# Optimization experiments

Hardware: AMD Instinct MI355X
Metric: run time of the kernel (lower is better)

## Reference

```python
import jax, jax.numpy as jnp
import numpy as np
from jax import lax

B, T, A, L, H, FD = 32, 64, 6, 32, 128, 256


def setup_inputs() -> dict:
    key = jax.random.key(0)
    ks = jax.random.split(key, 24)
    rn = lambda k, s, sc: jax.random.normal(k, s, jnp.float32) * sc
    return {
        "states": rn(ks[0], (B, T, 3, 64, 64), 1.0),
        "actions": rn(ks[1], (B, T, A), 1.0),
        # CNN encoder params (scale ~ 1/sqrt(fan_in))
        "c1_w": rn(ks[2], (32, 3, 4, 4), 0.14), "c1_b": rn(ks[3], (32,), 0.01),
        "c2_w": rn(ks[4], (64, 32, 4, 4), 0.044), "c2_b": rn(ks[5], (64,), 0.01),
        "c3_w": rn(ks[6], (128, 64, 4, 4), 0.031), "c3_b": rn(ks[7], (128,), 0.01),
        "c4_w": rn(ks[8], (256, 128, 4, 4), 0.022), "c4_b": rn(ks[9], (256,), 0.01),
        "fc_w": rn(ks[10], (FD, 256 * 4 * 4), 0.0156), "fc_b": rn(ks[11], (FD,), 0.01),
        # GRUCell params (torch layout: W_ih (3H, in), W_hh (3H, H))
        "gru_wih": rn(ks[12], (3 * H, L + A), 0.16), "gru_whh": rn(ks[13], (3 * H, H), 0.088),
        "gru_bih": rn(ks[14], (3 * H,), 0.01), "gru_bhh": rn(ks[15], (3 * H,), 0.01),
        "prior_w": rn(ks[16], (2 * L, H), 0.088), "prior_b": rn(ks[17], (2 * L,), 0.01),
        "post_w": rn(ks[18], (2 * L, H + FD), 0.05), "post_b": rn(ks[19], (2 * L,), 0.01),
        # reparameterization noise (randn_like in torch), one per (b, t)
        "eps": rn(ks[20], (B, T, L), 1.0),
    }


def _conv(x, w, b):
    # Conv2d(k=4, stride=2, pad=1), NCHW/OIHW
    y = lax.conv_general_dilated(x, w, window_strides=(2, 2),
                                 padding=[(1, 1), (1, 1)],
                                 dimension_numbers=("NCHW", "OIHW", "NCHW"))
    return jax.nn.relu(y + b[None, :, None, None])


def _encode(x, c1_w, c1_b, c2_w, c2_b, c3_w, c3_b, c4_w, c4_b, fc_w, fc_b):
    # x: (N, 3, 64, 64) -> (N, FD)
    x = _conv(x, c1_w, c1_b)
    x = _conv(x, c2_w, c2_b)
    x = _conv(x, c3_w, c3_b)
    x = _conv(x, c4_w, c4_b)  # (N, 256, 4, 4)
    x = x.reshape(x.shape[0], -1)
    return x @ fc_w.T + fc_b


def _gru_cell(x, h, wih, whh, bih, bhh):
    gi = x @ wih.T + bih
    gh = h @ whh.T + bhh
    i_r, i_z, i_n = jnp.split(gi, 3, axis=-1)
    h_r, h_z, h_n = jnp.split(gh, 3, axis=-1)
    r = jax.nn.sigmoid(i_r + h_r)
    z = jax.nn.sigmoid(i_z + h_z)
    n = jnp.tanh(i_n + r * h_n)
    return (1.0 - z) * n + z * h


def reference(states, actions, c1_w, c1_b, c2_w, c2_b, c3_w, c3_b, c4_w, c4_b,
              fc_w, fc_b, gru_wih, gru_whh, gru_bih, gru_bhh,
              prior_w, prior_b, post_w, post_b, eps):
    b, t = states.shape[0], states.shape[1]
    # encoder has no recurrent dependency: encode all frames at once
    feats = _encode(states.reshape(b * t, *states.shape[2:]),
                    c1_w, c1_b, c2_w, c2_b, c3_w, c3_b, c4_w, c4_b,
                    fc_w, fc_b).reshape(b, t, -1)  # (B, T, FD)

    def step(carry, inp):
        h, z = carry
        a_t, f_t, e_t = inp
        h = _gru_cell(jnp.concatenate([z, a_t], -1), h,
                      gru_wih, gru_whh, gru_bih, gru_bhh)
        mu_p, lv_p = jnp.split(h @ prior_w.T + prior_b, 2, axis=-1)
        mu_q, lv_q = jnp.split(jnp.concatenate([h, f_t], -1) @ post_w.T + post_b, 2, axis=-1)
        z = mu_q + jnp.exp(0.5 * lv_q) * e_t
        return (h, z), (mu_p, lv_p, mu_q, lv_q, h, z)

    h0 = jnp.zeros((b, gru_whh.shape[1]), states.dtype)
    z0 = jnp.zeros((b, prior_w.shape[0] // 2), states.dtype)
    xs = (jnp.swapaxes(actions, 0, 1), jnp.swapaxes(feats, 0, 1),
          jnp.swapaxes(eps, 0, 1))
    _, ys = lax.scan(step, (h0, z0), xs)
    # (T, B, d) -> (B, T, d)
    return tuple(jnp.swapaxes(y, 0, 1) for y in ys)
```

## Files before the change

### kernel.cpp

```cpp
#include <hip/hip_runtime.h>
#include <math.h>

#define Bn 32
#define Tn 64
#define An 6
#define Ln 32
#define Hn 128
#define FDn 256
#define Nimg (Bn*Tn)

typedef __attribute__((ext_vector_type(8))) short frag_ab;
typedef __attribute__((ext_vector_type(4))) float frag_cd;
typedef _Float16 h2_t __attribute__((ext_vector_type(2)));

__device__ __forceinline__ float sigmoid_fast(float x){
  return __builtin_amdgcn_rcpf(1.f + __expf(-x));
}
__device__ __forceinline__ float tanh_fast(float x){
  float x2 = fminf(fmaxf(2.f*x, -30.f), 30.f);
  float e = __expf(x2);
  return (e - 1.f) * __builtin_amdgcn_rcpf(e + 1.f);
}

__device__ __forceinline__ unsigned short f2bf(float f){
  unsigned int u = __float_as_uint(f);
  unsigned int r = (u + 0x7fffu + ((u >> 16) & 1u)) >> 16;
  return (unsigned short)r;
}
__device__ __forceinline__ unsigned packh(float a, float b){
  union { h2_t h; unsigned u; } x;
  x.h = (h2_t){(_Float16)a, (_Float16)b};
  return x.u;
}
__device__ __forceinline__ float fdot2u(unsigned a, unsigned b, float c){
  union { unsigned u; h2_t h; } ua, ub;
  ua.u = a; ub.u = b;
#if __has_builtin(__builtin_amdgcn_fdot2)
  return __builtin_amdgcn_fdot2(ua.h, ub.h, c, false);
#else
  return c + (float)ua.h.x*(float)ub.h.x + (float)ua.h.y*(float)ub.h.y;
#endif
}
#define BAR_LDS() asm volatile("s_waitcnt lgkmcnt(0)\n\ts_barrier" ::: "memory")

__device__ __forceinline__ int swz_w(int r, int p){
  return ((r >> 4) << 9) + (p << 7) + ((((r & 15) ^ (p << 2))) << 3);
}
__device__ __forceinline__ int swz_r(int f, int l){
  return (f << 9) + ((l >> 4) << 7) + ((((l & 15) ^ ((l >> 4) << 2))) << 3);
}

__global__ void __launch_bounds__(256)
states_nhwc_kernel(const float* __restrict__ src, unsigned short* __restrict__ dst)
{
  int idx = blockIdx.x*256 + threadIdx.x;
  int n = idx >> 12, pix = idx & 4095;
  const float* s = src + (size_t)n*3*4096 + pix;
  union { unsigned short e[4]; uint2 v; } u;
  u.e[0] = f2bf(s[0]); u.e[1] = f2bf(s[4096]); u.e[2] = f2bf(s[8192]); u.e[3] = 0;
  *(uint2*)(dst + (size_t)idx*4) = u.v;
}

__global__ void __launch_bounds__(256)
prep2_kernel(const float* __restrict__ c1w, const float* __restrict__ c2w,
             const float* __restrict__ c3w, const float* __restrict__ c4w,
             const float* __restrict__ fcw,
             const float* __restrict__ gwhh, const float* __restrict__ gwih,
             const float* __restrict__ prw,  const float* __restrict__ pow_,
             unsigned short* __restrict__ w1p, unsigned short* __restrict__ w2p,
             unsigned short* __restrict__ w3p, unsigned short* __restrict__ w4p,
             unsigned short* __restrict__ wfcp,
             unsigned* __restrict__ g_whh2, unsigned* __restrict__ g_wihz,
             unsigned* __restrict__ g_pr2,  unsigned* __restrict__ g_po2)
{
  const int bid = blockIdx.x, tid = threadIdx.x;
  if (bid < 128){
    int idx = bid*256+tid;
    int k = idx >> 9, r = idx & 511, tap = r >> 5, c = r & 31;
    w2p[idx] = f2bf(c2w[k*512 + c*16 + tap]);
  } else if (bid < 640){
    int idx = (bid-128)*256+tid;
    int k = idx >> 10, r = idx & 1023, tap = r >> 6, c = r & 63;
    w3p[idx] = f2bf(c3w[k*1024 + c*16 + tap]);
  } else if (bid < 2688){
    int idx = (bid-640)*256+tid;
    int k = idx >> 11, r = idx & 2047, tap = r >> 7, c = r & 127;
    w4p[idx] = f2bf(c4w[k*2048 + c*16 + tap]);
  } else if (bid < 6784){
    int idx = (bid-2688)*256+tid;
    int o = idx >> 12, r = idx & 4095, sp = r >> 8, c = r & 255;
    wfcp[idx] = f2bf(fcw[o*4096 + c*16 + sp]);
  } else if (bid < 6792){
    int idx = (bid-6784)*256+tid;
    int k = idx >> 6, r = idx & 63, tap = r >> 2, c = r & 3;
    w1p[idx] = (c < 3) ? f2bf(c1w[k*48 + c*16 + tap]) : (unsigned short)0;
  } else if (bid < 6888){
    int idx = (bid-6792)*256+tid;
    int c = idx / 384, i = idx - c*384;
    g_whh2[idx] = packh(gwhh[i*128 + 2*c], gwhh[i*128 + 2*c + 1]);
  } else if (bid < 6912){
    int idx = (bid-6888)*256+tid;
    int c = idx / 384, i = idx - c*384;
    g_wihz[idx] = packh(gwih[i*38 + 2*c], gwih[i*38 + 2*c + 1]);
  } else if (bid < 6928){
    int idx = (bid-6912)*256+tid;
    int c = idx >> 6, o = idx & 63;
    g_pr2[idx] = packh(prw[o*128 + 2*c], prw[o*128 + 2*c + 1]);
  } else {
    int idx = (bid-6928)*256+tid;
    int c = idx >> 6, o = idx & 63;
    g_po2[idx] = packh(pow_[o*384 + 2*c], pow_[o*384 + 2*c + 1]);
  }
}

__global__ void __launch_bounds__(384)
gia_kernel(const float* __restrict__ actions, const float* __restrict__ gwih,
           const float* __restrict__ bih, float* __restrict__ GIA)
{
  const int tid = threadIdx.x;
  const int bt0 = blockIdx.x * 8;
  __shared__ float ash[48];
  if (tid < 48) ash[tid] = actions[(size_t)bt0*6 + tid];
  float w6[6];
#pragma unroll
  for (int k = 0; k < 6; k++) w6[k] = gwih[tid*38 + 32 + k];
  const float bv = bih[tid];
  __syncthreads();
#pragma unroll
  for (int r = 0; r < 8; r++){
    float v = bv;
#pragma unroll
    for (int k = 0; k < 6; k++) v = fmaf(ash[r*6+k], w6[k], v);
    GIA[(size_t)(bt0 + r)*384 + tid] = v;
  }
}

__global__ void __launch_bounds__(256)
pof_kernel(const float* __restrict__ feats, const float* __restrict__ po_w,
           const float* __restrict__ po_b, float* __restrict__ POF)
{
  const int tid = threadIdx.x;
  const int bt0 = blockIdx.x * 8;
  __shared__ __align__(16) float fsh[8*256];
  const float4* fsrc = (const float4*)(feats + (size_t)bt0*256);
  ((float4*)fsh)[tid]       = fsrc[tid];
  ((float4*)fsh)[tid + 256] = fsrc[tid + 256];
  __syncthreads();
  const float4* w4 = (const float4*)po_w;
  const float4* f4 = (const float4*)fsh;
#pragma unroll
  for (int i = 0; i < 2; i++){
    int item = tid + i*256;
    int row = item >> 6, o = item & 63;
    float4 acc = {0.f,0.f,0.f,0.f};
#pragma unroll 8
    for (int k = 0; k < 64; k++){
      float4 wv = w4[o*96 + 32 + k];
      float4 fv = f4[row*64 + k];
      acc.x = fmaf(wv.x, fv.x, acc.x);
      acc.y = fmaf(wv.y, fv.y, acc.y);
      acc.z = fmaf(wv.z, fv.z, acc.z);
      acc.w = fmaf(wv.w, fv.w, acc.w);
    }
    POF[(size_t)(bt0 + row)*64 + o] = (acc.x + acc.y) + (acc.z + acc.w) + po_b[o];
  }
}

template<int Cin, int IN, int Kout, int OUT, int BN, int LOG_SPB>
__global__ void __launch_bounds__(256)
convN_mfma(const unsigned short* __restrict__ in,
           const unsigned short* __restrict__ wB,
           const float* __restrict__ bias,
           unsigned short* __restrict__ out)
{
  constexpr int SPB = OUT*OUT;
  constexpr int KD  = 16*Cin;
  constexpr int NCH = KD/32;
  constexpr int NFN = BN/32;
  constexpr int BFR = BN/16;
  constexpr int BSL = (BN*4 + 255)/256;
  __shared__ __align__(16) unsigned short Alds[2][8*512];
  __shared__ __align__(16) unsigned short Blds[2][BFR*512];

  const int tid = threadIdx.x;
  const int wave = tid >> 6, lane = tid & 63;
  const unsigned m0 = blockIdx.x * 128;
  const int n0 = blockIdx.y * BN;

  const int p = tid & 3;
  const unsigned short* baseA[2]; int oyA[2], oxA[2]; int AdstI[2];
#pragma unroll
  for (int h = 0; h < 2; h++){
    int r = (tid >> 2) + h*64;
    unsigned m = m0 + r;
    int nimg = m >> LOG_SPB;
    int sp = m & (SPB - 1);
    oyA[h] = sp / OUT; oxA[h] = sp & (OUT - 1);
    baseA[h] = in + (size_t)nimg * IN * IN * Cin;
    AdstI[h] = swz_w(r, p);
  }

  const unsigned short* BsrcH[BSL]; int BdstIH[BSL]; bool bActH[BSL];
#pragma unroll
  for (int h = 0; h < BSL; h++){
    int bn = (tid >> 2) + h*64, pb = tid & 3;
    bActH[h] = bn < BN;
    BsrcH[h] = wB + (size_t)(n0 + bn)*KD + pb*8;
    BdstIH[h] = swz_w(bn, pb);
  }

  const int mhalf = wave >> 1, nhalf = wave & 1;
  frag_cd acc[4][NFN];
#pragma unroll
  for (int i = 0; i < 4; i++)
#pragma unroll
    for (int j = 0; j < NFN; j++) acc[i][j] = (frag_cd){0.f,0.f,0.f,0.f};

  auto loadA = [&](int kt, int h) -> uint4 {
    if constexpr (Cin >= 32){
      constexpr int CPT = Cin/32;
      int tap = kt / CPT;
      int c0 = (kt - tap*CPT)*32;
      int kh = tap >> 2, kw = tap & 3;
      int iy = 2*oyA[h] - 1 + kh;
      int ix = 2*oxA[h] - 1 + kw;
      uint4 v = {0u,0u,0u,0u};
      if ((unsigned)iy < (unsigned)IN && (unsigned)ix < (unsigned)IN)
        v = *(const uint4*)(baseA[h] + ((iy*IN + ix)*Cin + c0 + p*8));
      return v;
    } else {
      int kh = kt*2 + (p >> 1);
      int kw0 = (p & 1)*2;
      int iy = 2*oyA[h] - 1 + kh;
      int ix0 = 2*oxA[h] - 1 + kw0;
      union { uint2 u2[2]; uint4 u4; } v; v.u4 = (uint4){0u,0u,0u,0u};
      bool iyok = (unsigned)iy < (unsigned)IN;
      const unsigned short* rowp = baseA[h] + iy*IN*4;
#pragma unroll
      for (int d = 0; d < 2; d++){
        int ix = ix0 + d;
        if (iyok && (unsigned)ix < (unsigned)IN) v.u2[d] = *(const uint2*)(rowp + ix*4);
      }
      return v.u4;
    }
  };

  const int rdoff = swz_r(0, lane);

  uint4 aR0 = loadA(0,0), aR1 = loadA(0,1);
  uint4 bR[BSL];
#pragma unroll
  for (int h = 0; h < BSL; h++)
    bR[h] = bActH[h] ? *(const uint4*)BsrcH[h] : (uint4){0u,0u,0u,0u};
  *(uint4*)&Alds[0][AdstI[0]] = aR0;
  *(uint4*)&Alds[0][AdstI[1]] = aR1;
#pragma unroll
  for (int h = 0; h < BSL; h++)
    if (bActH[h]) *(uint4*)&Blds[0][BdstIH[h]] = bR[h];
  if (NCH > 1){
    aR0 = loadA(1,0); aR1 = loadA(1,1);
#pragma unroll
    for (int h = 0; h < BSL; h++)
      if (bActH[h]) bR[h] = *(const uint4*)(BsrcH[h] + 32);
  }
  BAR_LDS();

#pragma unroll 2
  for (int kt = 0; kt < NCH; kt++){
    const int cur = kt & 1, nxt = cur ^ 1;
    if (kt + 1 < NCH){
      *(uint4*)&Alds[nxt][AdstI[0]] = aR0;
      *(uint4*)&Alds[nxt][AdstI[1]] = aR1;
#pragma unroll
      for (int h = 0; h < BSL; h++)
        if (bActH[h]) *(uint4*)&Blds[nxt][BdstIH[h]] = bR[h];
      if (kt + 2 < NCH){
        aR0 = loadA(kt+2, 0);
        aR1 = loadA(kt+2, 1);
#pragma unroll
        for (int h = 0; h < BSL; h++)
          if (bActH[h]) bR[h] = *(const uint4*)(BsrcH[h] + (kt+2)*32);
      }
    }
    frag_ab a[4], bf[NFN];
#pragma unroll
    for (int i = 0; i < 4; i++)
      a[i] = *(const frag_ab*)&Alds[cur][(((mhalf<<2) + i) << 9) + rdoff];
#pragma unroll
    for (int j = 0; j < NFN; j++)
      bf[j] = *(const frag_ab*)&Blds[cur][((nhalf*NFN + j) << 9) + rdoff];
#pragma unroll
    for (int i = 0; i < 4; i++)
#pragma unroll
      for (int j = 0; j < NFN; j++)
        acc[i][j] = __builtin_amdgcn_mfma_f32_16x16x32_bf16(a[i], bf[j], acc[i][j], 0, 0, 0);
    BAR_LDS();
  }

  const unsigned mb = m0 + mhalf*64 + ((lane >> 4) << 2);
#pragma unroll
  for (int j = 0; j < NFN; j++){
    const int kg = n0 + nhalf*(NFN*16) + j*16 + (lane & 15);
    const float bv = bias[kg];
#pragma unroll
    for (int i = 0; i < 4; i++){
#pragma unroll
      for (int r = 0; r < 4; r++){
        unsigned mg = mb + i*16 + r;
        out[(size_t)mg*Kout + kg] = f2bf(fmaxf(acc[i][j][r] + bv, 0.f));
      }
    }
  }
}

__global__ void __launch_bounds__(256)
fc_mfma2(const unsigned short* __restrict__ A, const unsigned short* __restrict__ wB,
         const float* __restrict__ bias, float* __restrict__ outF)
{
  constexpr int KD = 4096, NCH = KD/32;
  __shared__ __align__(16) unsigned short Alds[2][4*512];
  __shared__ __align__(16) unsigned short Blds[2][4*512];

  const int tid = threadIdx.x, wave = tid >> 6, lane = tid & 63;
  const int m0 = blockIdx.x * 64, n0 = blockIdx.y * 64;
  const int r = tid >> 2, pc = tid & 3;
  const unsigned short* Asrc = A + (size_t)(m0 + r)*KD + pc*8;
  const unsigned short* Bsrc = wB + (size_t)(n0 + r)*KD + pc*8;
  const int wI = swz_w(r, pc);
  const int mh = wave >> 1, nh = wave & 1;
  const int rdoff = swz_r(0, lane);

  frag_cd acc[2][2];
#pragma unroll
  for (int i = 0; i < 2; i++)
#pragma unroll
    for (int j = 0; j < 2; j++) acc[i][j] = (frag_cd){0.f,0.f,0.f,0.f};

  uint4 aP = *(const uint4*)Asrc, bP = *(const uint4*)Bsrc;
  *(uint4*)&Alds[0][wI] = aP;
  *(uint4*)&Blds[0][wI] = bP;
  aP = *(const uint4*)(Asrc + 32);
  bP = *(const uint4*)(Bsrc + 32);
  BAR_LDS();

#pragma unroll 2
  for (int kt = 0; kt < NCH; kt++){
    const int cur = kt & 1, nxt = cur ^ 1;
    if (kt + 1 < NCH){
      *(uint4*)&Alds[nxt][wI] = aP;
      *(uint4*)&Blds[nxt][wI] = bP;
      if (kt + 2 < NCH){
        aP = *(const uint4*)(Asrc + (kt+2)*32);
        bP = *(const uint4*)(Bsrc + (kt+2)*32);
      }
    }
    frag_ab a[2], b[2];
#pragma unroll
    for (int i = 0; i < 2; i++) a[i] = *(const frag_ab*)&Alds[cur][(((mh<<1)+i) << 9) + rdoff];
#pragma unroll
    for (int j = 0; j < 2; j++) b[j] = *(const frag_ab*)&Blds[cur][(((nh<<1)+j) << 9) + rdoff];
#pragma unroll
    for (int i = 0; i < 2; i++)
#pragma unroll
      for (int j = 0; j < 2; j++)
        acc[i][j] = __builtin_amdgcn_mfma_f32_16x16x32_bf16(a[i], b[j], acc[i][j], 0, 0, 0);
    BAR_LDS();
  }

  const int mb = m0 + mh*32 + ((lane >> 4) << 2);
#pragma unroll
  for (int j = 0; j < 2; j++){
    const int kg = n0 + nh*32 + j*16 + (lane & 15);
    const float bv = bias[kg];
#pragma unroll
    for (int i = 0; i < 2; i++)
#pragma unroll
      for (int rr = 0; rr < 4; rr++)
        outF[(size_t)(mb + i*16 + rr)*256 + kg] = acc[i][j][rr] + bv;
  }
}

__global__ void __launch_bounds__(384)
rssm_scan7(const unsigned* __restrict__ g_whh2, const unsigned* __restrict__ g_wihz,
           const unsigned* __restrict__ g_pr2,  const unsigned* __restrict__ g_po2,
           const float* __restrict__ GIA, const float* __restrict__ POF,
           const float* __restrict__ eps, const float* __restrict__ bhh,
           const float* __restrict__ pr_b, float* __restrict__ out)
{
  __shared__ __align__(16) _Float16 sh_h[128];
  __shared__ __align__(16) _Float16 sh_z[32];
  __shared__ float sh_gi[384];
  __shared__ float sh_gh[384];
  __shared__ __align__(16) uint4 wpr4[16*64];
  __shared__ __align__(16) uint4 wpo4[16*64];

  const int b = blockIdx.x, tid = threadIdx.x;
  const int wv = tid >> 6, lane = tid & 63;

  unsigned whh2[64];
#pragma unroll
  for (int c = 0; c < 64; c++) whh2[c] = g_whh2[c*384 + tid];
  unsigned wihz[16];
#pragma unroll
  for (int c = 0; c < 16; c++) wihz[c] = g_wihz[c*384 + tid];
  const float bhh_i = bhh[tid];
  const float prbr = (wv == 0) ? pr_b[lane] : 0.f;

  for (int i = tid; i < 1024; i += 384){
    const int c4 = i >> 6, o = i & 63;
    wpr4[i] = (uint4){ g_pr2[(4*c4+0)*64 + o], g_pr2[(4*c4+1)*64 + o],
                       g_pr2[(4*c4+2)*64 + o], g_pr2[(4*c4+3)*64 + o] };
    wpo4[i] = (uint4){ g_po2[(4*c4+0)*64 + o], g_po2[(4*c4+1)*64 + o],
                       g_po2[(4*c4+2)*64 + o], g_po2[(4*c4+3)*64 + o] };
  }

  unsigned hsu[64];
#pragma unroll
  for (int c = 0; c < 64; c++) hsu[c] = 0u;

  if (tid < 128) sh_h[tid] = (_Float16)0.f;
  if (tid < 32)  sh_z[tid] = (_Float16)0.f;

  float GIAr = GIA[(size_t)(b*64)*384 + tid];
  float POFr = (wv == 1) ? POF[(size_t)(b*64)*64 + lane] : 0.f;
  float epsr = (wv == 1 && lane < 32) ? eps[(size_t)(b*64)*32 + lane] : 0.f;

  const int OFF_MUP = 0;
  const int OFF_LVP = Bn*Tn*Ln;
  const int OFF_MUQ = 2*Bn*Tn*Ln;
  const int OFF_LVQ = 3*Bn*Tn*Ln;
  const int OFF_H   = 4*Bn*Tn*Ln;
  const int OFF_Z   = 4*Bn*Tn*Ln + Bn*Tn*Hn;

  float hreg = 0.f;
  __syncthreads();

  for (int t = 0; t < Tn; t++){
    const size_t bt = (size_t)b*64 + t;

    {
      const uint4* Z4 = (const uint4*)sh_z;
      uint4 z0 = Z4[0], z1 = Z4[1], z2 = Z4[2], z3 = Z4[3];
      float a0 = GIAr, a1 = 0.f, a2 = 0.f, a3 = 0.f;
      a0 = fdot2u(wihz[0],  z0.x, a0); a1 = fdot2u(wihz[1],  z0.y, a1);
      a2 = fdot2u(wihz[2],  z0.z, a2); a3 = fdot2u(wihz[3],  z0.w, a3);
      a0 = fdot2u(wihz[4],  z1.x, a0); a1 = fdot2u(wihz[5],  z1.y, a1);
      a2 = fdot2u(wihz[6],  z1.z, a2); a3 = fdot2u(wihz[7],  z1.w, a3);
      a0 = fdot2u(wihz[8],  z2.x, a0); a1 = fdot2u(wihz[9],  z2.y, a1);
      a2 = fdot2u(wihz[10], z2.z, a2); a3 = fdot2u(wihz[11], z2.w, a3);
      a0 = fdot2u(wihz[12], z3.x, a0); a1 = fdot2u(wihz[13], z3.y, a1);
      a2 = fdot2u(wihz[14], z3.z, a2); a3 = fdot2u(wihz[15], z3.w, a3);

      float g0 = bhh_i, g1 = 0.f, g2 = 0.f, g3 = 0.f;
#pragma unroll
      for (int c = 0; c < 64; c += 4){
        g0 = fdot2u(whh2[c],   hsu[c],   g0);
        g1 = fdot2u(whh2[c+1], hsu[c+1], g1);
        g2 = fdot2u(whh2[c+2], hsu[c+2], g2);
        g3 = fdot2u(whh2[c+3], hsu[c+3], g3);
      }
      sh_gi[tid] = (a0 + a1) + (a2 + a3);
      sh_gh[tid] = (g0 + g1) + (g2 + g3);
    }
    if (t < Tn-1) GIAr = GIA[(bt+1)*384 + tid];
    BAR_LDS();

    if (tid < 128){
      const float r  = sigmoid_fast(sh_gi[tid]       + sh_gh[tid]);
      const float zg = sigmoid_fast(sh_gi[128 + tid] + sh_gh[128 + tid]);
      const float nn = tanh_fast(fmaf(r, sh_gh[256 + tid], sh_gi[256 + tid]));
      hreg = (1.f - zg)*nn + zg*hreg;
      sh_h[tid] = (_Float16)hreg;
      out[OFF_H + bt*128 + tid] = hreg;
    }
    BAR_LDS();

    {
      unsigned hv = ((const unsigned*)sh_h)[lane];
#pragma unroll
      for (int c = 0; c < 64; c++) hsu[c] = __builtin_amdgcn_readlane(hv, c);
    }
    if (wv == 0){
      float p0 = prbr, p1 = 0.f, p2 = 0.f, p3 = 0.f;
#pragma unroll
      for (int c4 = 0; c4 < 16; c4++){
        const uint4 w = wpr4[(c4 << 6) + lane];
        p0 = fdot2u(w.x, hsu[4*c4+0], p0);
        p1 = fdot2u(w.y, hsu[4*c4+1], p1);
        p2 = fdot2u(w.z, hsu[4*c4+2], p2);
        p3 = fdot2u(w.w, hsu[4*c4+3], p3);
      }
      const float p = (p0 + p1) + (p2 + p3);
      if (lane < 32) out[OFF_MUP + bt*32 + lane] = p;
      else           out[OFF_LVP + bt*32 + (lane - 32)] = p;
    } else if (wv == 1){
      float p0 = POFr, p1 = 0.f, p2 = 0.f, p3 = 0.f;
#pragma unroll
      for (int c4 = 0; c4 < 16; c4++){
        const uint4 w = wpo4[(c4 << 6) + lane];
        p0 = fdot2u(w.x, hsu[4*c4+0], p0);
        p1 = fdot2u(w.y, hsu[4*c4+1], p1);
        p2 = fdot2u(w.z, hsu[4*c4+2], p2);
        p3 = fdot2u(w.w, hsu[4*c4+3], p3);
      }
      const float p = (p0 + p1) + (p2 + p3);
      const float q = __shfl_xor(p, 32);
      if (lane < 32){
        out[OFF_MUQ + bt*32 + lane] = p;
        const float zz = fmaf(__expf(0.5f*q), epsr, p);
        sh_z[lane] = (_Float16)zz;
        out[OFF_Z + bt*32 + lane] = zz;
      } else {
        out[OFF_LVQ + bt*32 + (lane - 32)] = p;
      }
      if (t < Tn-1){
        POFr = POF[(bt+1)*64 + lane];
        if (lane < 32) epsr = eps[(bt+1)*32 + lane];
      }
    }
    BAR_LDS();
  }
}

extern "C" void kernel_launch(void* const* d_in, const int* in_sizes, int n_in,
                              void* d_out, int out_size, void* d_ws, size_t ws_size,
                              hipStream_t stream)
{
  const float* states = (const float*)d_in[0];
  const float* actions= (const float*)d_in[1];
  const float* c1_w = (const float*)d_in[2];  const float* c1_b = (const float*)d_in[3];
  const float* c2_w = (const float*)d_in[4];  const float* c2_b = (const float*)d_in[5];
  const float* c3_w = (const float*)d_in[6];  const float* c3_b = (const float*)d_in[7];
  const float* c4_w = (const float*)d_in[8];  const float* c4_b = (const float*)d_in[9];
  const float* fc_w = (const float*)d_in[10]; const float* fc_b = (const float*)d_in[11];
  const float* gwih = (const float*)d_in[12]; const float* gwhh = (const float*)d_in[13];
  const float* gbih = (const float*)d_in[14]; const float* gbhh = (const float*)d_in[15];
  const float* pr_w = (const float*)d_in[16]; const float* pr_b = (const float*)d_in[17];
  const float* po_w = (const float*)d_in[18]; const float* po_b = (const float*)d_in[19];
  const float* eps  = (const float*)d_in[20];

  char* p = (char*)d_ws;
  auto alloc = [&](size_t bytes){ char* r = p; p += (bytes + 255) & ~255ULL; return r; };

  unsigned short* statesB = (unsigned short*)alloc((size_t)Nimg*4096*4*2);
  unsigned short* act1    = (unsigned short*)alloc((size_t)Nimg*1024*32*2);
  unsigned short* act2    = (unsigned short*)alloc((size_t)Nimg*256*64*2);
  unsigned short* act3    = (unsigned short*)alloc((size_t)Nimg*64*128*2);
  unsigned short* act4    = (unsigned short*)alloc((size_t)Nimg*16*256*2);
  float*          feats   = (float*)alloc((size_t)Nimg*FDn*4);
  unsigned short* w1p     = (unsigned short*)alloc(32*64*2);
  unsigned short* w2p     = (unsigned short*)alloc((size_t)64*512*2);
  unsigned short* w3p     = (unsigned short*)alloc((size_t)128*1024*2);
  unsigned short* w4p     = (unsigned short*)alloc((size_t)256*2048*2);
  unsigned short* wfcp    = (unsigned short*)alloc((size_t)256*4096*2);
  unsigned* g_whh2 = (unsigned*)alloc((size_t)24576*4);
  unsigned* g_wihz = (unsigned*)alloc((size_t)6144*4);
  unsigned* g_pr2  = (unsigned*)alloc((size_t)4096*4);
  unsigned* g_po2  = (unsigned*)alloc((size_t)4096*4);
  float*    GIAb   = (float*)alloc((size_t)786432*4);
  float*    POFb   = (float*)alloc((size_t)Nimg*64*4);

  states_nhwc_kernel<<<Nimg*4096/256, 256, 0, stream>>>(states, statesB);
  prep2_kernel<<<6944, 256, 0, stream>>>(c1_w, c2_w, c3_w, c4_w, fc_w,
                                         gwhh, gwih, pr_w, po_w,
                                         w1p, w2p, w3p, w4p, wfcp,
                                         g_whh2, g_wihz, g_pr2, g_po2);
  gia_kernel<<<Nimg/8, 384, 0, stream>>>(actions, gwih, gbih, GIAb);

  convN_mfma<4,64,32,32,32,10>  <<< dim3(Nimg*1024/128, 1), 256, 0, stream >>>(statesB, w1p, c1_b, act1);
  convN_mfma<32,32,64,16,64,8>  <<< dim3(Nimg*256/128, 1), 256, 0, stream >>>(act1, w2p, c2_b, act2);
  convN_mfma<64,16,128,8,128,6> <<< dim3(Nimg*64/128, 1), 256, 0, stream >>>(act2, w3p, c3_b, act3);
  convN_mfma<128,8,256,4,128,4> <<< dim3(Nimg*16/128, 2), 256, 0, stream >>>(act3, w4p, c4_b, act4);

  fc_mfma2<<< dim3(Nimg/64, 4), 256, 0, stream >>>(act4, wfcp, fc_b, feats);
  pof_kernel<<< Nimg/8, 256, 0, stream >>>(feats, po_w, po_b, POFb);

  rssm_scan7<<< Bn, 384, 0, stream >>>(g_whh2, g_wihz, g_pr2, g_po2,
                                       GIAb, POFb, eps, gbhh, pr_b, (float*)d_out);
}
```

Measured before the change: 590.9 us.

## Move prior head out of scan and split GRU hidden weights between registers and LDS

Result: no change. 599.0 us (+1.4%).

```diff
diff --git a/kernel.cpp b/kernel.cpp
--- a/kernel.cpp
+++ b/kernel.cpp
@@ -66,12 +66,12 @@
              const float* __restrict__ c3w, const float* __restrict__ c4w,
              const float* __restrict__ fcw,
              const float* __restrict__ gwhh, const float* __restrict__ gwih,
-             const float* __restrict__ prw,  const float* __restrict__ pow_,
+             const float* __restrict__ pow_,
              unsigned short* __restrict__ w1p, unsigned short* __restrict__ w2p,
              unsigned short* __restrict__ w3p, unsigned short* __restrict__ w4p,
              unsigned short* __restrict__ wfcp,
              unsigned* __restrict__ g_whh2, unsigned* __restrict__ g_wihz,
-             unsigned* __restrict__ g_pr2,  unsigned* __restrict__ g_po2)
+             unsigned* __restrict__ g_po2)
 {
   const int bid = blockIdx.x, tid = threadIdx.x;
   if (bid < 128){
@@ -102,14 +102,12 @@
     int idx = (bid-6888)*256+tid;
     int c = idx / 384, i = idx - c*384;
     g_wihz[idx] = packh(gwih[i*38 + 2*c], gwih[i*38 + 2*c + 1]);
-  } else if (bid < 6928){
+  } else {
     int idx = (bid-6912)*256+tid;
-    int c = idx >> 6, o = idx & 63;
-    g_pr2[idx] = packh(prw[o*128 + 2*c], prw[o*128 + 2*c + 1]);
-  } else {
-    int idx = (bid-6928)*256+tid;
-    int c = idx >> 6, o = idx & 63;
-    g_po2[idx] = packh(pow_[o*384 + 2*c], pow_[o*384 + 2*c + 1]);
+    if (idx < 4096){
+      int c = idx >> 6, o = idx & 63;
+      g_po2[idx] = packh(pow_[o*384 + 2*c], pow_[o*384 + 2*c + 1]);
+    }
   }
 }
 
@@ -163,6 +161,41 @@
       acc.w = fmaf(wv.w, fv.w, acc.w);
     }
     POF[(size_t)(bt0 + row)*64 + o] = (acc.x + acc.y) + (acc.z + acc.w) + po_b[o];
+  }
+}
+
+__global__ void __launch_bounds__(256)
+prior_kernel(const float* __restrict__ hbuf, const float* __restrict__ prw,
+             const float* __restrict__ pr_b, float* __restrict__ out)
+{
+  const int OFF_MUP = 0;
+  const int OFF_LVP = Bn*Tn*Ln;
+  const int tid = threadIdx.x;
+  const int bt0 = blockIdx.x * 8;
+  __shared__ __align__(16) float hsh[8*128];
+  const float4* hsrc = (const float4*)(hbuf + (size_t)bt0*128);
+  ((float4*)hsh)[tid] = hsrc[tid];
+  __syncthreads();
+  const float4* w4 = (const float4*)prw;
+  const float4* h4 = (const float4*)hsh;
+#pragma unroll
+  for (int i = 0; i < 2; i++){
+    int item = tid + i*256;
+    int row = item >> 6, o = item & 63;
+    float4 acc = {0.f,0.f,0.f,0.f};
+#pragma unroll 8
+    for (int k = 0; k < 32; k++){
+      float4 wv = w4[o*32 + k];
+      float4 hv = h4[row*32 + k];
+      acc.x = fmaf(wv.x, hv.x, acc.x);
+      acc.y = fmaf(wv.y, hv.y, acc.y);
+      acc.z = fmaf(wv.z, hv.z, acc.z);
+      acc.w = fmaf(wv.w, hv.w, acc.w);
+    }
+    const float p = (acc.x + acc.y) + (acc.z + acc.w) + pr_b[o];
+    const size_t bt = (size_t)(bt0 + row);
+    if (o < 32) out[OFF_MUP + bt*32 + o] = p;
+    else        out[OFF_LVP + bt*32 + (o - 32)] = p;
   }
 }
 
@@ -381,35 +414,37 @@
 }
 
 __global__ void __launch_bounds__(384)
-rssm_scan7(const unsigned* __restrict__ g_whh2, const unsigned* __restrict__ g_wihz,
-           const unsigned* __restrict__ g_pr2,  const unsigned* __restrict__ g_po2,
+rssm_scan8(const unsigned* __restrict__ g_whh2, const unsigned* __restrict__ g_wihz,
+           const unsigned* __restrict__ g_po2,
            const float* __restrict__ GIA, const float* __restrict__ POF,
            const float* __restrict__ eps, const float* __restrict__ bhh,
-           const float* __restrict__ pr_b, float* __restrict__ out)
-{
+           float* __restrict__ out)
+{
+  __shared__ __align__(16) uint4 wHI[8*384];
+  __shared__ __align__(16) uint4 wpo4[16*64];
   __shared__ __align__(16) _Float16 sh_h[128];
   __shared__ __align__(16) _Float16 sh_z[32];
   __shared__ float sh_gi[384];
   __shared__ float sh_gh[384];
-  __shared__ __align__(16) uint4 wpr4[16*64];
-  __shared__ __align__(16) uint4 wpo4[16*64];
 
   const int b = blockIdx.x, tid = threadIdx.x;
   const int wv = tid >> 6, lane = tid & 63;
 
-  unsigned whh2[64];
-#pragma unroll
-  for (int c = 0; c < 64; c++) whh2[c] = g_whh2[c*384 + tid];
+  unsigned whhLO[32];
+#pragma unroll
+  for (int c = 0; c < 32; c++) whhLO[c] = g_whh2[c*384 + tid];
   unsigned wihz[16];
 #pragma unroll
   for (int c = 0; c < 16; c++) wihz[c] = g_wihz[c*384 + tid];
   const float bhh_i = bhh[tid];
-  const float prbr = (wv == 0) ? pr_b[lane] : 0.f;
-
+
+  for (int i = tid; i < 8*384; i += 384){
+    const int c4 = i / 384, n = i - c4*384;
+    wHI[i] = (uint4){ g_whh2[(32 + 4*c4 + 0)*384 + n], g_whh2[(32 + 4*c4 + 1)*384 + n],
+                      g_whh2[(32 + 4*c4 + 2)*384 + n], g_whh2[(32 + 4*c4 + 3)*384 + n] };
+  }
   for (int i = tid; i < 1024; i += 384){
     const int c4 = i >> 6, o = i & 63;
-    wpr4[i] = (uint4){ g_pr2[(4*c4+0)*64 + o], g_pr2[(4*c4+1)*64 + o],
-                       g_pr2[(4*c4+2)*64 + o], g_pr2[(4*c4+3)*64 + o] };
     wpo4[i] = (uint4){ g_po2[(4*c4+0)*64 + o], g_po2[(4*c4+1)*64 + o],
                        g_po2[(4*c4+2)*64 + o], g_po2[(4*c4+3)*64 + o] };
   }
@@ -422,11 +457,9 @@
   if (tid < 32)  sh_z[tid] = (_Float16)0.f;
 
   float GIAr = GIA[(size_t)(b*64)*384 + tid];
-  float POFr = (wv == 1) ? POF[(size_t)(b*64)*64 + lane] : 0.f;
-  float epsr = (wv == 1 && lane < 32) ? eps[(size_t)(b*64)*32 + lane] : 0.f;
-
-  const int OFF_MUP = 0;
-  const int OFF_LVP = Bn*Tn*Ln;
+  float POFr = (wv == 0) ? POF[(size_t)(b*64)*64 + lane] : 0.f;
+  float epsr = (wv == 0 && lane < 32) ? eps[(size_t)(b*64)*32 + lane] : 0.f;
+
   const int OFF_MUQ = 2*Bn*Tn*Ln;
   const int OFF_LVQ = 3*Bn*Tn*Ln;
   const int OFF_H   = 4*Bn*Tn*Ln;
@@ -439,25 +472,38 @@
     const size_t bt = (size_t)b*64 + t;
 
     {
-      const uint4* Z4 = (const uint4*)sh_z;
-      uint4 z0 = Z4[0], z1 = Z4[1], z2 = Z4[2], z3 = Z4[3];
+      unsigned zv = ((const unsigned*)sh_z)[lane & 15];
+      unsigned zsu[16];
+#pragma unroll
+      for (int c = 0; c < 16; c++) zsu[c] = __builtin_amdgcn_readlane(zv, c);
+
+      uint4 wh[8];
+#pragma unroll
+      for (int c4 = 0; c4 < 8; c4++) wh[c4] = wHI[c4*384 + tid];
+
       float a0 = GIAr, a1 = 0.f, a2 = 0.f, a3 = 0.f;
-      a0 = fdot2u(wihz[0],  z0.x, a0); a1 = fdot2u(wihz[1],  z0.y, a1);
-      a2 = fdot2u(wihz[2],  z0.z, a2); a3 = fdot2u(wihz[3],  z0.w, a3);
-      a0 = fdot2u(wihz[4],  z1.x, a0); a1 = fdot2u(wihz[5],  z1.y, a1);
-      a2 = fdot2u(wihz[6],  z1.z, a2); a3 = fdot2u(wihz[7],  z1.w, a3);
-      a0 = fdot2u(wihz[8],  z2.x, a0); a1 = fdot2u(wihz[9],  z2.y, a1);
-      a2 = fdot2u(wihz[10], z2.z, a2); a3 = fdot2u(wihz[11], z2.w, a3);
-      a0 = fdot2u(wihz[12], z3.x, a0); a1 = fdot2u(wihz[13], z3.y, a1);
-      a2 = fdot2u(wihz[14], z3.z, a2); a3 = fdot2u(wihz[15], z3.w, a3);
+#pragma unroll
+      for (int c = 0; c < 16; c += 4){
+        a0 = fdot2u(wihz[c],   zsu[c],   a0);
+        a1 = fdot2u(wihz[c+1], zsu[c+1], a1);
+        a2 = fdot2u(wihz[c+2], zsu[c+2], a2);
+        a3 = fdot2u(wihz[c+3], zsu[c+3], a3);
+      }
 
       float g0 = bhh_i, g1 = 0.f, g2 = 0.f, g3 = 0.f;
 #pragma unroll
-      for (int c = 0; c < 64; c += 4){
-        g0 = fdot2u(whh2[c],   hsu[c],   g0);
-        g1 = fdot2u(whh2[c+1], hsu[c+1], g1);
-        g2 = fdot2u(whh2[c+2], hsu[c+2], g2);
-        g3 = fdot2u(whh2[c+3], hsu[c+3], g3);
+      for (int c = 0; c < 32; c += 4){
+        g0 = fdot2u(whhLO[c],   hsu[c],   g0);
+        g1 = fdot2u(whhLO[c+1], hsu[c+1], g1);
+        g2 = fdot2u(whhLO[c+2], hsu[c+2], g2);
+        g3 = fdot2u(whhLO[c+3], hsu[c+3], g3);
+      }
+#pragma unroll
+      for (int c4 = 0; c4 < 8; c4++){
+        g0 = fdot2u(wh[c4].x, hsu[32 + 4*c4 + 0], g0);
+        g1 = fdot2u(wh[c4].y, hsu[32 + 4*c4 + 1], g1);
+        g2 = fdot2u(wh[c4].z, hsu[32 + 4*c4 + 2], g2);
+        g3 = fdot2u(wh[c4].w, hsu[32 + 4*c4 + 3], g3);
       }
       sh_gi[tid] = (a0 + a1) + (a2 + a3);
       sh_gh[tid] = (g0 + g1) + (g2 + g3);
@@ -481,19 +527,6 @@
       for (int c = 0; c < 64; c++) hsu[c] = __builtin_amdgcn_readlane(hv, c);
     }
     if (wv == 0){
-      float p0 = prbr, p1 = 0.f, p2 = 0.f, p3 = 0.f;
-#pragma unroll
-      for (int c4 = 0; c4 < 16; c4++){
-        const uint4 w = wpr4[(c4 << 6) + lane];
-        p0 = fdot2u(w.x, hsu[4*c4+0], p0);
-        p1 = fdot2u(w.y, hsu[4*c4+1], p1);
-        p2 = fdot2u(w.z, hsu[4*c4+2], p2);
-        p3 = fdot2u(w.w, hsu[4*c4+3], p3);
-      }
-      const float p = (p0 + p1) + (p2 + p3);
-      if (lane < 32) out[OFF_MUP + bt*32 + lane] = p;
-      else           out[OFF_LVP + bt*32 + (lane - 32)] = p;
-    } else if (wv == 1){
       float p0 = POFr, p1 = 0.f, p2 = 0.f, p3 = 0.f;
 #pragma unroll
       for (int c4 = 0; c4 < 16; c4++){
@@ -555,16 +588,15 @@
   unsigned short* wfcp    = (unsigned short*)alloc((size_t)256*4096*2);
   unsigned* g_whh2 = (unsigned*)alloc((size_t)24576*4);
   unsigned* g_wihz = (unsigned*)alloc((size_t)6144*4);
-  unsigned* g_pr2  = (unsigned*)alloc((size_t)4096*4);
   unsigned* g_po2  = (unsigned*)alloc((size_t)4096*4);
   float*    GIAb   = (float*)alloc((size_t)786432*4);
   float*    POFb   = (float*)alloc((size_t)Nimg*64*4);
 
   states_nhwc_kernel<<<Nimg*4096/256, 256, 0, stream>>>(states, statesB);
-  prep2_kernel<<<6944, 256, 0, stream>>>(c1_w, c2_w, c3_w, c4_w, fc_w,
-                                         gwhh, gwih, pr_w, po_w,
+  prep2_kernel<<<6928, 256, 0, stream>>>(c1_w, c2_w, c3_w, c4_w, fc_w,
+                                         gwhh, gwih, po_w,
                                          w1p, w2p, w3p, w4p, wfcp,
-                                         g_whh2, g_wihz, g_pr2, g_po2);
+                                         g_whh2, g_wihz, g_po2);
   gia_kernel<<<Nimg/8, 384, 0, stream>>>(actions, gwih, gbih, GIAb);
 
   convN_mfma<4,64,32,32,32,10>  <<< dim3(Nimg*1024/128, 1), 256, 0, stream >>>(statesB, w1p, c1_b, act1);
@@ -575,6 +607,9 @@
   fc_mfma2<<< dim3(Nimg/64, 4), 256, 0, stream >>>(act4, wfcp, fc_b, feats);
   pof_kernel<<< Nimg/8, 256, 0, stream >>>(feats, po_w, po_b, POFb);
 
-  rssm_scan7<<< Bn, 384, 0, stream >>>(g_whh2, g_wihz, g_pr2, g_po2,
-                                       GIAb, POFb, eps, gbhh, pr_b, (float*)d_out);
-}
+  rssm_scan8<<< Bn, 384, 0, stream >>>(g_whh2, g_wihz, g_po2,
+                                       GIAb, POFb, eps, gbhh, (float*)d_out);
+
+  float* hbuf = (float*)d_out + 4*Bn*Tn*Ln;
+  prior_kernel<<< Nimg/8, 256, 0, stream >>>(hbuf, pr_w, pr_b, (float*)d_out);
+}
```
